# Optimization experiments

Hardware: AMD Instinct MI355X
Metric: run time of the kernel (lower is better)

## Reference

```python
import jax, jax.numpy as jnp
import numpy as np

N, IN_DIM, HID, HEADS, HOPS, NCLS, E = 20000, 1536, 256, 4, 3, 3, 320000
HD = HID // HEADS
EPS = 1e-5
NEG_SLOPE = 0.2


def layer_norm(x, g, b):
    mu = jnp.mean(x, axis=-1, keepdims=True)
    var = jnp.var(x, axis=-1, keepdims=True)
    return (x - mu) * jax.lax.rsqrt(var + EPS) * g + b


def gatv2(x, src, dst, Wl, bl, Wr, br, att, bias):
    # x: [N, HID]; src/dst: [E'] (self loops included)
    xl = (x @ Wl + bl).reshape(N, HEADS, HD)  # source transform
    xr = (x @ Wr + br).reshape(N, HEADS, HD)  # target transform
    e = jax.nn.leaky_relu(xl[src] + xr[dst], NEG_SLOPE)          # [E', H, D]
    logits = jnp.einsum('ehd,hd->eh', e, att)                     # [E', H]
    m = jax.ops.segment_max(logits, dst, num_segments=N)         # [N, H]
    ex = jnp.exp(logits - m[dst])
    denom = jax.ops.segment_sum(ex, dst, num_segments=N)
    alpha = ex / denom[dst]                                       # softmax per dst
    msg = xl[src] * alpha[:, :, None]                             # [E', H, D]
    out = jax.ops.segment_sum(msg, dst, num_segments=N)
    return out.reshape(N, HID) + bias


def setup_inputs() -> dict:
    key = jax.random.key(0)
    ks = jax.random.split(key, 20)
    s = lambda k, shp, sc: jax.random.normal(k, shp, jnp.float32) * sc
    return {
        'features': s(ks[0], (N, IN_DIM), 1.0),
        'edge_index': jax.random.randint(ks[1], (2, E), 0, N, jnp.int64),
        'proj_W': s(ks[2], (IN_DIM, HID), 0.02),
        'proj_b': jnp.zeros((HID,), jnp.float32),
        'n0_g': jnp.ones((HID,), jnp.float32),
        'n0_b': jnp.zeros((HID,), jnp.float32),
        'Wl': s(ks[3], (HOPS, HID, HID), 0.05),
        'bl': jnp.zeros((HOPS, HID), jnp.float32),
        'Wr': s(ks[4], (HOPS, HID, HID), 0.05),
        'br': jnp.zeros((HOPS, HID), jnp.float32),
        'att': s(ks[5], (HOPS, HEADS, HD), 0.1),
        'gbias': jnp.zeros((HOPS, HID), jnp.float32),
        'ln_g': jnp.ones((HOPS, HID), jnp.float32),
        'ln_b': jnp.zeros((HOPS, HID), jnp.float32),
        'h1_W': s(ks[6], (HID, HID), 0.05),
        'h1_b': jnp.zeros((HID,), jnp.float32),
        'h2_W': s(ks[7], (HID, NCLS), 0.05),
        'h2_b': jnp.zeros((NCLS,), jnp.float32),
    }


def reference(features, edge_index, proj_W, proj_b, n0_g, n0_b, Wl, bl, Wr, br,
              att, gbias, ln_g, ln_b, h1_W, h1_b, h2_W, h2_b):
    # add self loops (PyG GATv2Conv default)
    loop = jnp.arange(N, dtype=edge_index.dtype)
    src = jnp.concatenate([edge_index[0], loop])
    dst = jnp.concatenate([edge_index[1], loop])

    x = layer_norm(features @ proj_W + proj_b, n0_g, n0_b)
    for h in range(HOPS):
        g = gatv2(x, src, dst, Wl[h], bl[h], Wr[h], br[h], att[h], gbias[h])
        x = layer_norm(g + x, ln_g[h], ln_b[h])
    # head (dropout inactive at eval); torch GELU is exact erf form
    x = jax.nn.gelu(x @ h1_W + h1_b, approximate=False)
    return x @ h2_W + h2_b
```

## Files before the change

kernel.cpp:

```cpp
#include <hip/hip_runtime.h>
#include <hip/hip_bf16.h>
#include <math.h>

#define NN 20000
#define MPAD 20096
#define INDIM 1536
#define HID 256
#define NE 320000
#define NEDGE (NE + NN)
#define EPSV 1e-5f
#define NEG 0.2f

typedef unsigned short ushort_b;
typedef unsigned int uint32;
typedef __bf16 bf16x8 __attribute__((ext_vector_type(8)));
typedef float f32x4 __attribute__((ext_vector_type(4)));

#define AS1(p) ((const __attribute__((address_space(1))) void*)(p))
#define AS3(p) ((__attribute__((address_space(3))) void*)(p))

__device__ inline ushort_b f2bf(float x) {
  union { float f; uint32 u; } v; v.f = x;
  uint32 r = v.u + 0x7FFFu + ((v.u >> 16) & 1u);
  return (ushort_b)(r >> 16);
}
__device__ inline float bf2f(ushort_b h) {
  union { uint32 u; float f; } v; v.u = ((uint32)h) << 16;
  return v.f;
}
__device__ inline float4 ldbf4(const ushort_b* p) {
  ushort4 u = *(const ushort4*)p;
  float4 f;
  f.x = bf2f(u.x); f.y = bf2f(u.y); f.z = bf2f(u.z); f.w = bf2f(u.w);
  return f;
}

template<int AFP32, int OUTMODE>
__global__ __launch_bounds__(256) void gemm_mfma(
    const void* __restrict__ Av,
    const ushort_b* __restrict__ Bt0, const ushort_b* __restrict__ Bt1,
    const float* __restrict__ bias0, const float* __restrict__ bias1,
    void* __restrict__ C0, void* __restrict__ C1,
    int Mstore, int Kloop, int Kstride, int kb0, int kb1)
{
  __shared__ ushort_b As0[128 * 32], As1[128 * 32];
  __shared__ ushort_b Bs0[128 * 32], Bs1[128 * 32];
  const ushort_b* Bt = blockIdx.z ? Bt1 : Bt0;
  const float* bias  = blockIdx.z ? bias1 : bias0;
  void* Cv           = blockIdx.z ? C1 : C0;
  int kbase          = blockIdx.z ? kb1 : kb0;

  int tid = threadIdx.x;
  int wave = tid >> 6, lane = tid & 63;
  int r0 = blockIdx.y * 128;
  int c0 = blockIdx.x * 128;
  int wm = (wave >> 1) << 6, wn = (wave & 1) << 6;
  int mrow = lane & 15, quad = lane >> 4;
  int nk = Kloop >> 5;

  const float* Af = (const float*)Av;
  const ushort_b* Ab = (const ushort_b*)Av;

  f32x4 acc[4][4] = {};
  float4 pA0[4], pA1[4];

  auto issueB = [&](int k0, ushort_b* lds) {
#pragma unroll
    for (int it = 0; it < 2; it++) {
      int off = (wave << 10) + (it << 12) + (lane << 4);
      int row = off >> 6, colb = off & 63;
      const char* g = (const char*)Bt + ((size_t)(c0 + row) * Kstride + kbase + k0) * 2 + colb;
      __builtin_amdgcn_global_load_lds(AS1(g), AS3((char*)lds + off), 16, 0, 0);
    }
  };
  auto issueA = [&](int k0, ushort_b* lds) {
#pragma unroll
    for (int it = 0; it < 2; it++) {
      int off = (wave << 10) + (it << 12) + (lane << 4);
      int row = off >> 6, colb = off & 63;
      const char* g = (const char*)Ab + ((size_t)(r0 + row) * Kstride + kbase + k0) * 2 + colb;
      __builtin_amdgcn_global_load_lds(AS1(g), AS3((char*)lds + off), 16, 0, 0);
    }
  };
  auto loadA = [&](int k0, float4* dst) {
#pragma unroll
    for (int p = 0; p < 4; p++) {
      int off4 = (p << 8) + tid;
      int row = off4 >> 3, col4 = off4 & 7;
      int grow = r0 + row;
      dst[p] = (grow < Mstore)
          ? *(const float4*)(Af + (size_t)grow * Kstride + kbase + k0 + (col4 << 2))
          : make_float4(0.f, 0.f, 0.f, 0.f);
    }
  };
  auto writeA = [&](const float4* src, ushort_b* lds) {
#pragma unroll
    for (int p = 0; p < 4; p++) {
      int off4 = (p << 8) + tid;
      int row = off4 >> 3, col4 = off4 & 7;
      uint2 u;
      u.x = (uint32)f2bf(src[p].x) | ((uint32)f2bf(src[p].y) << 16);
      u.y = (uint32)f2bf(src[p].z) | ((uint32)f2bf(src[p].w) << 16);
      *(uint2*)(lds + (row << 5) + (col4 << 2)) = u;
    }
  };
  auto computeStage = [&](const ushort_b* Asb, const ushort_b* Bsb) {
    bf16x8 af[4], bfr[4];
#pragma unroll
    for (int t = 0; t < 4; t++) {
      af[t]  = *(const bf16x8*)(Asb + ((wm + (t << 4) + mrow) << 5) + (quad << 3));
      bfr[t] = *(const bf16x8*)(Bsb + ((wn + (t << 4) + mrow) << 5) + (quad << 3));
    }
#pragma unroll
    for (int mt = 0; mt < 4; mt++)
#pragma unroll
      for (int nt = 0; nt < 4; nt++)
        acc[mt][nt] = __builtin_amdgcn_mfma_f32_16x16x32_bf16(af[mt], bfr[nt], acc[mt][nt], 0, 0, 0);
  };

  if (AFP32) {
    loadA(0, pA0);
    issueB(0, Bs0);
    loadA(32, pA1);
    writeA(pA0, As0);
  } else {
    issueA(0, As0);
    issueB(0, Bs0);
  }

  for (int k = 0; k < nk; k += 2) {
    __syncthreads();
    if (k + 1 < nk) {
      issueB((k + 1) << 5, Bs1);
      if (AFP32) {
        writeA(pA1, As1);
        if (k + 2 < nk) loadA((k + 2) << 5, pA0);
      } else {
        issueA((k + 1) << 5, As1);
      }
    }
    computeStage(As0, Bs0);
    __syncthreads();
    if (k + 2 < nk) {
      issueB((k + 2) << 5, Bs0);
      if (AFP32) {
        writeA(pA0, As0);
        if (k + 3 < nk) loadA((k + 3) << 5, pA1);
      } else {
        issueA((k + 2) << 5, As0);
      }
    }
    computeStage(As1, Bs1);
  }

#pragma unroll
  for (int nt = 0; nt < 4; nt++) {
    int col = c0 + wn + (nt << 4) + mrow;
    float bb = bias[col];
#pragma unroll
    for (int mt = 0; mt < 4; mt++) {
#pragma unroll
      for (int r = 0; r < 4; r++) {
        int row = r0 + wm + (mt << 4) + (quad << 2) + r;
        if (row < Mstore) {
          float v = acc[mt][nt][r] + bb;
          if (OUTMODE == 3) v = 0.5f * v * (1.f + erff(v * 0.70710678118654752f));
          if (OUTMODE == 0) ((float*)Cv)[(size_t)row * 256 + col] = v;
          else              ((ushort_b*)Cv)[(size_t)row * 256 + col] = f2bf(v);
        }
      }
    }
  }
}

__global__ __launch_bounds__(256) void transpose_cast(
    const float* __restrict__ in, ushort_b* __restrict__ out, int R, int C)
{
  __shared__ float t[32][33];
  int bx = blockIdx.x * 32;
  int by = blockIdx.y * 32;
  for (int i = threadIdx.y; i < 32; i += 8)
    t[i][threadIdx.x] = in[(size_t)(by + i) * C + bx + threadIdx.x];
  __syncthreads();
  for (int i = threadIdx.y; i < 32; i += 8)
    out[(size_t)(bx + i) * R + by + threadIdx.x] = f2bf(t[threadIdx.x][i]);
}

__global__ __launch_bounds__(256) void ln_sum_kernel(
    const float* __restrict__ in0, const float* __restrict__ in1,
    const float* __restrict__ g, const float* __restrict__ b,
    float* __restrict__ out, ushort_b* __restrict__ bf_out, int n)
{
  int wave = threadIdx.x >> 6, lane = threadIdx.x & 63;
  int row = blockIdx.x * 4 + wave;
  if (row >= n) return;
  int c = lane << 2;
  float4 v = *(const float4*)(in0 + (size_t)row * HID + c);
  float4 v1 = *(const float4*)(in1 + (size_t)row * HID + c);
  v.x += v1.x; v.y += v1.y; v.z += v1.z; v.w += v1.w;
  float s1 = v.x + v.y + v.z + v.w;
  float s2 = v.x * v.x + v.y * v.y + v.z * v.z + v.w * v.w;
#pragma unroll
  for (int m = 1; m < 64; m <<= 1) {
    s1 += __shfl_xor(s1, m, 64);
    s2 += __shfl_xor(s2, m, 64);
  }
  float mu = s1 * (1.f / 256.f);
  float var = s2 * (1.f / 256.f) - mu * mu;
  float rstd = rsqrtf(var + EPSV);
  float4 gv = *(const float4*)(g + c);
  float4 bv = *(const float4*)(b + c);
  float4 o;
  o.x = (v.x - mu) * rstd * gv.x + bv.x;
  o.y = (v.y - mu) * rstd * gv.y + bv.y;
  o.z = (v.z - mu) * rstd * gv.z + bv.z;
  o.w = (v.w - mu) * rstd * gv.w + bv.w;
  *(float4*)(out + (size_t)row * HID + c) = o;
  ushort4 ub;
  ub.x = f2bf(o.x); ub.y = f2bf(o.y); ub.z = f2bf(o.z); ub.w = f2bf(o.w);
  *(ushort4*)(bf_out + (size_t)row * HID + c) = ub;
}

__global__ void count_kernel(const int* __restrict__ ei, int* __restrict__ cnt)
{
  int e = blockIdx.x * blockDim.x + threadIdx.x;
  if (e < NEDGE) {
    int d = (e < NE) ? ei[NE + e] : (e - NE);
    atomicAdd(&cnt[d], 1);
  }
}

__global__ __launch_bounds__(1024) void scan_kernel(
    const int* __restrict__ cnt, int* __restrict__ offs, int* __restrict__ cursor)
{
  __shared__ int sums[1024];
  int tid = threadIdx.x;
  const int CH = 20;
  int base = tid * CH;
  int loc[CH];
  int s = 0;
#pragma unroll
  for (int i = 0; i < CH; i++) {
    int idx = base + i;
    int v = (idx < NN) ? cnt[idx] : 0;
    loc[i] = s;
    s += v;
  }
  sums[tid] = s;
  __syncthreads();
  for (int off = 1; off < 1024; off <<= 1) {
    int t = (tid >= off) ? sums[tid - off] : 0;
    __syncthreads();
    sums[tid] += t;
    __syncthreads();
  }
  int pre = (tid == 0) ? 0 : sums[tid - 1];
#pragma unroll
  for (int i = 0; i < CH; i++) {
    int idx = base + i;
    if (idx < NN) { int e = pre + loc[i]; offs[idx] = e; cursor[idx] = e; }
  }
  if (tid == 0) offs[NN] = NEDGE;
}

__global__ void scatter_kernel(const int* __restrict__ ei, int* __restrict__ cursor,
                               int* __restrict__ csr_src)
{
  int e = blockIdx.x * blockDim.x + threadIdx.x;
  if (e < NEDGE) {
    int s, d;
    if (e < NE) { s = ei[e]; d = ei[NE + e]; }
    else { s = e - NE; d = e - NE; }
    int p = atomicAdd(&cursor[d], 1);
    csr_src[p] = s;
  }
}

__device__ inline float edge_logit(float4 xv, float4 xrv, float4 attv) {
  float e0 = xv.x + xrv.x, e1 = xv.y + xrv.y, e2 = xv.z + xrv.z, e3 = xv.w + xrv.w;
  e0 = (e0 > 0.f) ? e0 : NEG * e0;
  e1 = (e1 > 0.f) ? e1 : NEG * e1;
  e2 = (e2 > 0.f) ? e2 : NEG * e2;
  e3 = (e3 > 0.f) ? e3 : NEG * e3;
  float lc = e0 * attv.x + e1 * attv.y + e2 * attv.z + e3 * attv.w;
  lc += __shfl_xor(lc, 1, 16);
  lc += __shfl_xor(lc, 2, 16);
  lc += __shfl_xor(lc, 4, 16);
  lc += __shfl_xor(lc, 8, 16);
  return lc;
}

#define ACCUM(i, lg, xv) {                          \
    float w = __expf(lg);                            \
    lS[i] += w;                                      \
    pS##i##0 += w * xv.x; pS##i##1 += w * xv.y;      \
    pS##i##2 += w * xv.z; pS##i##3 += w * xv.w; }

__global__ __launch_bounds__(256) void gat_kernel(
    const ushort_b* __restrict__ xl, const ushort_b* __restrict__ xr,
    const float* __restrict__ x_in, const float* __restrict__ att,
    const float* __restrict__ gbias, const float* __restrict__ ln_g,
    const float* __restrict__ ln_b, const int* __restrict__ offs,
    const int* __restrict__ csr_src, float* __restrict__ x_out,
    ushort_b* __restrict__ xb_out)
{
  int wave = threadIdx.x >> 6, lane = threadIdx.x & 63;
  int node = blockIdx.x * 4 + wave;
  if (node >= NN) return;
  int c = lane << 2;
  float4 xrv = ldbf4(xr + (size_t)node * HID + c);
  float4 attv = *(const float4*)(att + c);

  float lS[4] = {0.f, 0.f, 0.f, 0.f};
  float pS00 = 0.f, pS01 = 0.f, pS02 = 0.f, pS03 = 0.f;
  float pS10 = 0.f, pS11 = 0.f, pS12 = 0.f, pS13 = 0.f;
  float pS20 = 0.f, pS21 = 0.f, pS22 = 0.f, pS23 = 0.f;
  float pS30 = 0.f, pS31 = 0.f, pS32 = 0.f, pS33 = 0.f;

  int e = offs[node], end = offs[node + 1];
  for (; e + 3 < end; e += 4) {
    int s0 = csr_src[e], s1 = csr_src[e + 1], s2 = csr_src[e + 2], s3 = csr_src[e + 3];
    float4 x0v = ldbf4(xl + (size_t)s0 * HID + c);
    float4 x1v = ldbf4(xl + (size_t)s1 * HID + c);
    float4 x2v = ldbf4(xl + (size_t)s2 * HID + c);
    float4 x3v = ldbf4(xl + (size_t)s3 * HID + c);
    float g0 = edge_logit(x0v, xrv, attv);
    float g1 = edge_logit(x1v, xrv, attv);
    float g2 = edge_logit(x2v, xrv, attv);
    float g3 = edge_logit(x3v, xrv, attv);
    ACCUM(0, g0, x0v);
    ACCUM(1, g1, x1v);
    ACCUM(2, g2, x2v);
    ACCUM(3, g3, x3v);
  }
  for (; e < end; e++) {
    int s0 = csr_src[e];
    float4 x0v = ldbf4(xl + (size_t)s0 * HID + c);
    float g0 = edge_logit(x0v, xrv, attv);
    ACCUM(0, g0, x0v);
  }

  float l = lS[0] + lS[1] + lS[2] + lS[3];
  float inv = 1.f / l;
  float a0 = (pS00 + pS10 + pS20 + pS30) * inv;
  float a1 = (pS01 + pS11 + pS21 + pS31) * inv;
  float a2 = (pS02 + pS12 + pS22 + pS32) * inv;
  float a3 = (pS03 + pS13 + pS23 + pS33) * inv;

  float4 xv = *(const float4*)(x_in + (size_t)node * HID + c);
  float4 gb = *(const float4*)(gbias + c);
  float o0 = a0 + gb.x + xv.x;
  float o1 = a1 + gb.y + xv.y;
  float o2 = a2 + gb.z + xv.z;
  float o3 = a3 + gb.w + xv.w;
  float s1s = o0 + o1 + o2 + o3;
  float s2s = o0 * o0 + o1 * o1 + o2 * o2 + o3 * o3;
#pragma unroll
  for (int mmk = 1; mmk < 64; mmk <<= 1) {
    s1s += __shfl_xor(s1s, mmk, 64);
    s2s += __shfl_xor(s2s, mmk, 64);
  }
  float mu = s1s * (1.f / 256.f);
  float var = s2s * (1.f / 256.f) - mu * mu;
  float rstd = rsqrtf(var + EPSV);
  float4 gv = *(const float4*)(ln_g + c);
  float4 bv = *(const float4*)(ln_b + c);
  float4 o;
  o.x = (o0 - mu) * rstd * gv.x + bv.x;
  o.y = (o1 - mu) * rstd * gv.y + bv.y;
  o.z = (o2 - mu) * rstd * gv.z + bv.z;
  o.w = (o3 - mu) * rstd * gv.w + bv.w;
  *(float4*)(x_out + (size_t)node * HID + c) = o;
  ushort4 ub;
  ub.x = f2bf(o.x); ub.y = f2bf(o.y); ub.z = f2bf(o.z); ub.w = f2bf(o.w);
  *(ushort4*)(xb_out + (size_t)node * HID + c) = ub;
}

__global__ __launch_bounds__(256) void head2_kernel(
    const ushort_b* __restrict__ t1, const float* __restrict__ W,
    const float* __restrict__ bias, float* __restrict__ out)
{
  int wave = threadIdx.x >> 6, lane = threadIdx.x & 63;
  int row = blockIdx.x * 4 + wave;
  if (row >= NN) return;
  int c = lane << 2;
  float4 v = ldbf4(t1 + (size_t)row * HID + c);
  float p0 = 0.f, p1 = 0.f, p2 = 0.f;
#pragma unroll
  for (int j = 0; j < 4; j++) {
    float vj = (&v.x)[j];
    p0 += vj * W[(c + j) * 3 + 0];
    p1 += vj * W[(c + j) * 3 + 1];
    p2 += vj * W[(c + j) * 3 + 2];
  }
#pragma unroll
  for (int mm = 1; mm < 64; mm <<= 1) {
    p0 += __shfl_xor(p0, mm, 64);
    p1 += __shfl_xor(p1, mm, 64);
    p2 += __shfl_xor(p2, mm, 64);
  }
  if (lane == 0) {
    out[(size_t)row * 3 + 0] = p0 + bias[0];
    out[(size_t)row * 3 + 1] = p1 + bias[1];
    out[(size_t)row * 3 + 2] = p2 + bias[2];
  }
}

extern "C" void kernel_launch(void* const* d_in, const int* in_sizes, int n_in,
                              void* d_out, int out_size, void* d_ws, size_t ws_size,
                              hipStream_t stream)
{
  const float* features = (const float*)d_in[0];
  const int*   ei       = (const int*)d_in[1];
  const float* proj_W   = (const float*)d_in[2];
  const float* proj_b   = (const float*)d_in[3];
  const float* n0_g     = (const float*)d_in[4];
  const float* n0_b     = (const float*)d_in[5];
  const float* Wl       = (const float*)d_in[6];
  const float* bl       = (const float*)d_in[7];
  const float* Wr       = (const float*)d_in[8];
  const float* br       = (const float*)d_in[9];
  const float* att      = (const float*)d_in[10];
  const float* gbias    = (const float*)d_in[11];
  const float* ln_g     = (const float*)d_in[12];
  const float* ln_b     = (const float*)d_in[13];
  const float* h1_W     = (const float*)d_in[14];
  const float* h1_b     = (const float*)d_in[15];
  const float* h2_W     = (const float*)d_in[16];
  const float* h2_b     = (const float*)d_in[17];
  float* out = (float*)d_out;

  char* w = (char*)d_ws;
  float*    x0    = (float*)w;    w += (size_t)NN * HID * 4;
  float*    x1    = (float*)w;    w += (size_t)NN * HID * 4;
  float*    part1 = (float*)w;    w += (size_t)NN * HID * 4;
  ushort_b* xlb   = (ushort_b*)w; w += (size_t)NN * HID * 2;
  ushort_b* xrb   = (ushort_b*)w; w += (size_t)NN * HID * 2;
  ushort_b* xb    = (ushort_b*)w; w += (size_t)MPAD * HID * 2;
  ushort_b* wtp   = (ushort_b*)w; w += (size_t)HID * INDIM * 2;
  ushort_b* wtl   = (ushort_b*)w; w += (size_t)3 * HID * HID * 2;
  ushort_b* wtr   = (ushort_b*)w; w += (size_t)3 * HID * HID * 2;
  ushort_b* wth1  = (ushort_b*)w; w += (size_t)HID * HID * 2;
  float* zbias = (float*)w; w += (size_t)HID * 4;
  int* cnt     = (int*)w;  w += (size_t)NN * 4;
  int* offs    = (int*)w;  w += (size_t)(NN + 1) * 4;
  int* cursor  = (int*)w;  w += (size_t)NN * 4;
  int* csr     = (int*)w;  w += (size_t)NEDGE * 4;

  hipMemsetAsync(cnt, 0, (size_t)NN * 4, stream);
  hipMemsetAsync(zbias, 0, (size_t)HID * 4, stream);
  hipMemsetAsync(xb + (size_t)NN * HID, 0, (size_t)(MPAD - NN) * HID * 2, stream);
  count_kernel<<<(NEDGE + 255) / 256, 256, 0, stream>>>(ei, cnt);
  scan_kernel<<<1, 1024, 0, stream>>>(cnt, offs, cursor);
  scatter_kernel<<<(NEDGE + 255) / 256, 256, 0, stream>>>(ei, cursor, csr);

  transpose_cast<<<dim3(HID / 32, INDIM / 32), dim3(32, 8), 0, stream>>>(proj_W, wtp, INDIM, HID);
  for (int h = 0; h < 3; h++) {
    transpose_cast<<<dim3(HID / 32, HID / 32), dim3(32, 8), 0, stream>>>(
        Wl + (size_t)h * HID * HID, wtl + (size_t)h * HID * HID, HID, HID);
    transpose_cast<<<dim3(HID / 32, HID / 32), dim3(32, 8), 0, stream>>>(
        Wr + (size_t)h * HID * HID, wtr + (size_t)h * HID * HID, HID, HID);
  }
  transpose_cast<<<dim3(HID / 32, HID / 32), dim3(32, 8), 0, stream>>>(h1_W, wth1, HID, HID);

  dim3 gsplit(2, MPAD / 128, 2);
  dim3 gsingle(2, MPAD / 128, 1);

  gemm_mfma<1, 0><<<gsplit, 256, 0, stream>>>(
      features, wtp, wtp, proj_b, zbias, x1, part1, NN, INDIM / 2, INDIM, 0, INDIM / 2);
  ln_sum_kernel<<<(NN + 3) / 4, 256, 0, stream>>>(x1, part1, n0_g, n0_b, x0, xb, NN);

  float* xcur = x0;
  float* xnxt = x1;
  for (int h = 0; h < 3; h++) {
    gemm_mfma<0, 2><<<gsplit, 256, 0, stream>>>(
        xb, wtl + (size_t)h * HID * HID, wtr + (size_t)h * HID * HID,
        bl + h * HID, br + h * HID, xlb, xrb, NN, HID, HID, 0, 0);
    gat_kernel<<<(NN + 3) / 4, 256, 0, stream>>>(
        xlb, xrb, xcur, att + h * HID, gbias + h * HID,
        ln_g + h * HID, ln_b + h * HID, offs, csr, xnxt, xb);
    float* t = xcur; xcur = xnxt; xnxt = t;
  }

  gemm_mfma<0, 3><<<gsingle, 256, 0, stream>>>(
      xb, wth1, wth1, h1_b, h1_b, xlb, xlb, NN, HID, HID, 0, 0);
  head2_kernel<<<(NN + 3) / 4, 256, 0, stream>>>(xlb, h2_W, h2_b, out);
}
```

Before: 566.8 us.

## Halve GEMM M-tile, split GAT edge lists across two waves, batch weight transposes

The GEMM tile shrinks from 128x128 to 64x128 rows per block. Each wave now owns a 32-column strip across all 64 rows, so the grid doubles for better occupancy and balance on the many compute units. The GAT kernel assigns two waves per destination node, each covering half of the incoming edges, and merges partial softmax sums through shared memory. This shortens each wave's serial gather chain but adds a block barrier and LDS traffic. The seven small weight transposes are also fused into one launch to cut launch overhead.

```diff
diff --git a/kernel.cpp b/kernel.cpp
--- a/kernel.cpp
+++ b/kernel.cpp
@@ -43,7 +43,7 @@
     void* __restrict__ C0, void* __restrict__ C1,
     int Mstore, int Kloop, int Kstride, int kb0, int kb1)
 {
-  __shared__ ushort_b As0[128 * 32], As1[128 * 32];
+  __shared__ ushort_b As0[64 * 32], As1[64 * 32];
   __shared__ ushort_b Bs0[128 * 32], Bs1[128 * 32];
   const ushort_b* Bt = blockIdx.z ? Bt1 : Bt0;
   const float* bias  = blockIdx.z ? bias1 : bias0;
@@ -52,17 +52,17 @@
 
   int tid = threadIdx.x;
   int wave = tid >> 6, lane = tid & 63;
-  int r0 = blockIdx.y * 128;
+  int r0 = blockIdx.y * 64;
   int c0 = blockIdx.x * 128;
-  int wm = (wave >> 1) << 6, wn = (wave & 1) << 6;
+  int wn = wave << 5;
   int mrow = lane & 15, quad = lane >> 4;
   int nk = Kloop >> 5;
 
   const float* Af = (const float*)Av;
   const ushort_b* Ab = (const ushort_b*)Av;
 
-  f32x4 acc[4][4] = {};
-  float4 pA0[4], pA1[4];
+  f32x4 acc[4][2] = {};
+  float4 pA0[2], pA1[2];
 
   auto issueB = [&](int k0, ushort_b* lds) {
 #pragma unroll
@@ -74,17 +74,14 @@
     }
   };
   auto issueA = [&](int k0, ushort_b* lds) {
-#pragma unroll
-    for (int it = 0; it < 2; it++) {
-      int off = (wave << 10) + (it << 12) + (lane << 4);
-      int row = off >> 6, colb = off & 63;
-      const char* g = (const char*)Ab + ((size_t)(r0 + row) * Kstride + kbase + k0) * 2 + colb;
-      __builtin_amdgcn_global_load_lds(AS1(g), AS3((char*)lds + off), 16, 0, 0);
-    }
+    int off = tid << 4;
+    int row = off >> 6, colb = off & 63;
+    const char* g = (const char*)Ab + ((size_t)(r0 + row) * Kstride + kbase + k0) * 2 + colb;
+    __builtin_amdgcn_global_load_lds(AS1(g), AS3((char*)lds + off), 16, 0, 0);
   };
   auto loadA = [&](int k0, float4* dst) {
 #pragma unroll
-    for (int p = 0; p < 4; p++) {
+    for (int p = 0; p < 2; p++) {
       int off4 = (p << 8) + tid;
       int row = off4 >> 3, col4 = off4 & 7;
       int grow = r0 + row;
@@ -95,7 +92,7 @@
   };
   auto writeA = [&](const float4* src, ushort_b* lds) {
 #pragma unroll
-    for (int p = 0; p < 4; p++) {
+    for (int p = 0; p < 2; p++) {
       int off4 = (p << 8) + tid;
       int row = off4 >> 3, col4 = off4 & 7;
       uint2 u;
@@ -105,17 +102,18 @@
     }
   };
   auto computeStage = [&](const ushort_b* Asb, const ushort_b* Bsb) {
-    bf16x8 af[4], bfr[4];
-#pragma unroll
-    for (int t = 0; t < 4; t++) {
-      af[t]  = *(const bf16x8*)(Asb + ((wm + (t << 4) + mrow) << 5) + (quad << 3));
-      bfr[t] = *(const bf16x8*)(Bsb + ((wn + (t << 4) + mrow) << 5) + (quad << 3));
-    }
-#pragma unroll
-    for (int mt = 0; mt < 4; mt++)
-#pragma unroll
-      for (int nt = 0; nt < 4; nt++)
-        acc[mt][nt] = __builtin_amdgcn_mfma_f32_16x16x32_bf16(af[mt], bfr[nt], acc[mt][nt], 0, 0, 0);
+    bf16x8 af[4], bfr[2];
+#pragma unroll
+    for (int t = 0; t < 4; t++)
+      af[t] = *(const bf16x8*)(Asb + (((t << 4) + mrow) << 5) + (quad << 3));
+#pragma unroll
+    for (int u = 0; u < 2; u++)
+      bfr[u] = *(const bf16x8*)(Bsb + ((wn + (u << 4) + mrow) << 5) + (quad << 3));
+#pragma unroll
+    for (int t = 0; t < 4; t++)
+#pragma unroll
+      for (int u = 0; u < 2; u++)
+        acc[t][u] = __builtin_amdgcn_mfma_f32_16x16x32_bf16(af[t], bfr[u], acc[t][u], 0, 0, 0);
   };
 
   if (AFP32) {
@@ -154,16 +152,16 @@
   }
 
 #pragma unroll
-  for (int nt = 0; nt < 4; nt++) {
-    int col = c0 + wn + (nt << 4) + mrow;
+  for (int u = 0; u < 2; u++) {
+    int col = c0 + wn + (u << 4) + mrow;
     float bb = bias[col];
 #pragma unroll
-    for (int mt = 0; mt < 4; mt++) {
+    for (int t = 0; t < 4; t++) {
 #pragma unroll
       for (int r = 0; r < 4; r++) {
-        int row = r0 + wm + (mt << 4) + (quad << 2) + r;
+        int row = r0 + (t << 4) + (quad << 2) + r;
         if (row < Mstore) {
-          float v = acc[mt][nt][r] + bb;
+          float v = acc[t][u][r] + bb;
           if (OUTMODE == 3) v = 0.5f * v * (1.f + erff(v * 0.70710678118654752f));
           if (OUTMODE == 0) ((float*)Cv)[(size_t)row * 256 + col] = v;
           else              ((ushort_b*)Cv)[(size_t)row * 256 + col] = f2bf(v);
@@ -184,6 +182,25 @@
   __syncthreads();
   for (int i = threadIdx.y; i < 32; i += 8)
     out[(size_t)(bx + i) * R + by + threadIdx.x] = f2bf(t[threadIdx.x][i]);
+}
+
+__global__ __launch_bounds__(256) void transpose7(
+    const float* __restrict__ Wl, const float* __restrict__ Wr,
+    const float* __restrict__ h1W, ushort_b* __restrict__ dst_base)
+{
+  int z = blockIdx.z;
+  const float* in = (z < 3) ? Wl + (size_t)z * 65536
+                  : (z < 6) ? Wr + (size_t)(z - 3) * 65536
+                            : h1W;
+  ushort_b* out = dst_base + (size_t)z * 65536;
+  __shared__ float t[32][33];
+  int bx = blockIdx.x * 32;
+  int by = blockIdx.y * 32;
+  for (int i = threadIdx.y; i < 32; i += 8)
+    t[i][threadIdx.x] = in[(size_t)(by + i) * 256 + bx + threadIdx.x];
+  __syncthreads();
+  for (int i = threadIdx.y; i < 32; i += 8)
+    out[(size_t)(bx + i) * 256 + by + threadIdx.x] = f2bf(t[threadIdx.x][i]);
 }
 
 __global__ __launch_bounds__(256) void ln_sum_kernel(
@@ -304,9 +321,10 @@
     const int* __restrict__ csr_src, float* __restrict__ x_out,
     ushort_b* __restrict__ xb_out)
 {
+  __shared__ float gbuf[2][64][5];
   int wave = threadIdx.x >> 6, lane = threadIdx.x & 63;
-  int node = blockIdx.x * 4 + wave;
-  if (node >= NN) return;
+  int nib = wave >> 1, sub = wave & 1;
+  int node = blockIdx.x * 2 + nib;
   int c = lane << 2;
   float4 xrv = ldbf4(xr + (size_t)node * HID + c);
   float4 attv = *(const float4*)(att + c);
@@ -317,8 +335,11 @@
   float pS20 = 0.f, pS21 = 0.f, pS22 = 0.f, pS23 = 0.f;
   float pS30 = 0.f, pS31 = 0.f, pS32 = 0.f, pS33 = 0.f;
 
-  int e = offs[node], end = offs[node + 1];
-  for (; e + 3 < end; e += 4) {
+  int beg = offs[node], end = offs[node + 1];
+  int mid = beg + ((end - beg + 1) >> 1);
+  int e  = sub ? mid : beg;
+  int e1 = sub ? end : mid;
+  for (; e + 3 < e1; e += 4) {
     int s0 = csr_src[e], s1 = csr_src[e + 1], s2 = csr_src[e + 2], s3 = csr_src[e + 3];
     float4 x0v = ldbf4(xl + (size_t)s0 * HID + c);
     float4 x1v = ldbf4(xl + (size_t)s1 * HID + c);
@@ -333,26 +354,42 @@
     ACCUM(2, g2, x2v);
     ACCUM(3, g3, x3v);
   }
-  for (; e < end; e++) {
+  for (; e < e1; e++) {
     int s0 = csr_src[e];
     float4 x0v = ldbf4(xl + (size_t)s0 * HID + c);
     float g0 = edge_logit(x0v, xrv, attv);
     ACCUM(0, g0, x0v);
   }
 
-  float l = lS[0] + lS[1] + lS[2] + lS[3];
+  float l  = lS[0] + lS[1] + lS[2] + lS[3];
+  float q0 = pS00 + pS10 + pS20 + pS30;
+  float q1 = pS01 + pS11 + pS21 + pS31;
+  float q2 = pS02 + pS12 + pS22 + pS32;
+  float q3 = pS03 + pS13 + pS23 + pS33;
+
+  if (sub) {
+    gbuf[nib][lane][0] = l;
+    gbuf[nib][lane][1] = q0;
+    gbuf[nib][lane][2] = q1;
+    gbuf[nib][lane][3] = q2;
+    gbuf[nib][lane][4] = q3;
+  }
+  __syncthreads();
+  if (sub) return;
+
+  l  += gbuf[nib][lane][0];
+  q0 += gbuf[nib][lane][1];
+  q1 += gbuf[nib][lane][2];
+  q2 += gbuf[nib][lane][3];
+  q3 += gbuf[nib][lane][4];
+
   float inv = 1.f / l;
-  float a0 = (pS00 + pS10 + pS20 + pS30) * inv;
-  float a1 = (pS01 + pS11 + pS21 + pS31) * inv;
-  float a2 = (pS02 + pS12 + pS22 + pS32) * inv;
-  float a3 = (pS03 + pS13 + pS23 + pS33) * inv;
-
   float4 xv = *(const float4*)(x_in + (size_t)node * HID + c);
   float4 gb = *(const float4*)(gbias + c);
-  float o0 = a0 + gb.x + xv.x;
-  float o1 = a1 + gb.y + xv.y;
-  float o2 = a2 + gb.z + xv.z;
-  float o3 = a3 + gb.w + xv.w;
+  float o0 = q0 * inv + gb.x + xv.x;
+  float o1 = q1 * inv + gb.y + xv.y;
+  float o2 = q2 * inv + gb.z + xv.z;
+  float o3 = q3 * inv + gb.w + xv.w;
   float s1s = o0 + o1 + o2 + o3;
   float s2s = o0 * o0 + o1 * o1 + o2 * o2 + o3 * o3;
 #pragma unroll
@@ -455,16 +492,10 @@
   scatter_kernel<<<(NEDGE + 255) / 256, 256, 0, stream>>>(ei, cursor, csr);
 
   transpose_cast<<<dim3(HID / 32, INDIM / 32), dim3(32, 8), 0, stream>>>(proj_W, wtp, INDIM, HID);
-  for (int h = 0; h < 3; h++) {
-    transpose_cast<<<dim3(HID / 32, HID / 32), dim3(32, 8), 0, stream>>>(
-        Wl + (size_t)h * HID * HID, wtl + (size_t)h * HID * HID, HID, HID);
-    transpose_cast<<<dim3(HID / 32, HID / 32), dim3(32, 8), 0, stream>>>(
-        Wr + (size_t)h * HID * HID, wtr + (size_t)h * HID * HID, HID, HID);
-  }
-  transpose_cast<<<dim3(HID / 32, HID / 32), dim3(32, 8), 0, stream>>>(h1_W, wth1, HID, HID);
-
-  dim3 gsplit(2, MPAD / 128, 2);
-  dim3 gsingle(2, MPAD / 128, 1);
+  transpose7<<<dim3(8, 8, 7), dim3(32, 8), 0, stream>>>(Wl, Wr, h1_W, wtl);
+
+  dim3 gsplit(2, MPAD / 64, 2);
+  dim3 gsingle(2, MPAD / 64, 1);
 
   gemm_mfma<1, 0><<<gsplit, 256, 0, stream>>>(
       features, wtp, wtp, proj_b, zbias, x1, part1, NN, INDIM / 2, INDIM, 0, INDIM / 2);
@@ -476,7 +507,7 @@
     gemm_mfma<0, 2><<<gsplit, 256, 0, stream>>>(
         xb, wtl + (size_t)h * HID * HID, wtr + (size_t)h * HID * HID,
         bl + h * HID, br + h * HID, xlb, xrb, NN, HID, HID, 0, 0);
-    gat_kernel<<<(NN + 3) / 4, 256, 0, stream>>>(
+    gat_kernel<<<NN / 2, 256, 0, stream>>>(
         xlb, xrb, xcur, att + h * HID, gbias + h * HID,
         ln_g + h * HID, ln_b + h * HID, offs, csr, xnxt, xb);
     float* t = xcur; xcur = xnxt; xnxt = t;
```

New measurement: 560.1 us. No clear change (-1.2%).
